# Performance work log

Hardware: AMD Instinct MI355X
Metric: run time of the kernel (lower is better)

## Reference

```python
import jax, jax.numpy as jnp
import numpy as np

K, S, P, NQ, NREPS = 3, 1, 1, 9, 2  # kernel, stride, pad, num_qubits, num_qreps


def _extract_patches(x, k, s):
    # x: (b, c, H, W) -> (b, c, ho, wo, k*k), patch elems in (kh, kw) row-major order
    b, c, H, W = x.shape
    ho = (H - k) // s + 1
    wo = (W - k) // s + 1
    cols = [x[:, :, i:i + (ho - 1) * s + 1:s, j:j + (wo - 1) * s + 1:s]
            for i in range(k) for j in range(k)]
    return jnp.stack(cols, axis=-1), ho, wo


def _cnot(state, c, t):
    # state: (N, 2, ..., 2); CNOT with control wire c, target wire t (wire q -> axis q+1)
    s0, s1 = jnp.split(state, 2, axis=c + 1)
    return jnp.concatenate([s0, jnp.flip(s1, axis=t + 1)], axis=c + 1)


def _simulate(angles, weights):
    # AngleEmbedding(RX) + BasicEntanglerLayers(RZ, CNOT ring) + expval(PauliY_i)
    # angles: (N, n) float; weights: (L, n) float -> (N, n) float expvals
    N, n = angles.shape
    half = 0.5 * angles
    # RX(theta)|0> = cos(t/2)|0> - i sin(t/2)|1>  (product state)
    vecs = jnp.stack([jnp.cos(half).astype(jnp.complex64),
                      -1j * jnp.sin(half)], axis=-1)  # (N, n, 2)
    state = vecs[:, 0]
    for q in range(1, n):
        state = state[..., None] * vecs[:, q].reshape((N,) + (1,) * q + (2,))
    # state: (N, 2, ..., 2), wire 0 = axis 1 (most significant)
    for l in range(weights.shape[0]):
        # RZ layer = single diagonal of shape (2,)*n, shared across patches
        pv = jnp.stack([jnp.exp(-0.5j * weights[l]),
                        jnp.exp(0.5j * weights[l])], axis=-1).astype(jnp.complex64)  # (n,2)
        diag = pv[0]
        for q in range(1, n):
            diag = diag[..., None] * pv[q].reshape((1,) * q + (2,))
        state = state * diag
        # CNOT ring (i -> i+1 mod n), as in BasicEntanglerLayers for n > 2
        for i in range(n):
            state = _cnot(state, i, (i + 1) % n)
    # <Y_i> = 2 * Im( sum conj(psi_{qi=0}) * psi_{qi=1} )
    exps = []
    for i in range(n):
        a, bdim = 1 << i, 1 << (n - 1 - i)
        r = state.reshape(N, a, 2, bdim)
        z = jnp.sum(jnp.conj(r[:, :, 0, :]) * r[:, :, 1, :], axis=(1, 2))
        exps.append(2.0 * z.imag)
    return jnp.stack(exps, axis=1)  # (N, n) float32


def setup_inputs() -> dict:
    key = jax.random.key(0)
    k1, k2 = jax.random.split(key)
    x = jax.random.uniform(k1, (16, 1, 28, 28), dtype=jnp.float32)
    weights = jax.random.uniform(k2, (NREPS, NQ), dtype=jnp.float32,
                                 minval=0.0, maxval=2.0 * np.pi)
    return {"x": x, "weights": weights}


def reference(x, weights):
    b = x.shape[0]
    xp = jnp.pad(x, ((0, 0), (0, 0), (P, P), (P, P)))
    patches, ho, wo = _extract_patches(xp, K, S)  # (b, 1, ho, wo, k*k)
    flat = patches.reshape(-1, NQ)                # (b*ho*wo, 9)  (c == 1)
    qout = _simulate(flat, weights)               # (b*ho*wo, 9)
    qout = qout.reshape(b, ho, wo, NQ)
    return qout.transpose(0, 3, 1, 2)             # (b, 9, ho, wo)
```

## Files before the change

kernel.cpp:

```cpp
#include <hip/hip_runtime.h>
#include <math.h>

#define NQ 9
#define NREPS 2
#define NB 512
#define NSIMS (16*28*28)

__host__ __device__ constexpr int csigma(int b) {
    for (int c = NQ - 1; c >= 0; --c) {
        const int t  = (c + 1) % NQ;
        const int pc = NQ - 1 - c;
        const int pt = NQ - 1 - t;
        b ^= ((b >> pc) & 1) << pt;
    }
    return b;
}
__host__ __device__ constexpr int csig2(int b) { return csigma(csigma(b)); }

constexpr int VB_[6] = { csig2(1<<0), csig2(1<<1), csig2(1<<2),
                         csig2(1<<3), csig2(1<<4), csig2(1<<5) };
constexpr int VR_[8] = { csig2(0<<6), csig2(1<<6), csig2(2<<6), csig2(3<<6),
                         csig2(4<<6), csig2(5<<6), csig2(6<<6), csig2(7<<6) };

template<int CTRL>
__device__ __forceinline__ float dppmov(float x) {
    return __int_as_float(__builtin_amdgcn_update_dpp(
        0, __float_as_int(x), CTRL, 0xF, 0xF, true));
}
template<int OFF>
__device__ __forceinline__ int swzx_i(int x) {
    return __builtin_amdgcn_ds_swizzle(x, OFF);
}
__device__ __forceinline__ float wave_reduce(float v) {
    v += dppmov<0x111>(v);
    v += dppmov<0x112>(v);
    v += dppmov<0x114>(v);
    v += dppmov<0x118>(v);
    v += dppmov<0x142>(v);
    v += dppmov<0x143>(v);
    return v;
}

typedef __fp16 h2_t __attribute__((ext_vector_type(2)));
__device__ __forceinline__ int packf16(float a, float b) {
    h2_t h = __builtin_amdgcn_cvt_pkrtz(a, b);
    int i; __builtin_memcpy(&i, &h, 4); return i;
}
__device__ __forceinline__ float2 unpackf16(int i) {
    h2_t h; __builtin_memcpy(&h, &i, 4);
    return make_float2((float)h.x, (float)h.y);
}

__global__ __launch_bounds__(256) void quanv_fused(
    const float* __restrict__ x,
    const float* __restrict__ w,
    float* __restrict__ out)
{
    __shared__ float2 T[NB];
    {
        const int t = threadIdx.x;
        #pragma unroll
        for (int bb = t; bb < NB; bb += 256) {
            float th = 0.f;
            int cur = bb;
            #pragma unroll
            for (int l = NREPS - 1; l >= 0; --l) {
                cur = csigma(cur);
                #pragma unroll
                for (int q = 0; q < NQ; ++q) {
                    const float wq = 0.5f * w[l * NQ + q];
                    th += ((cur >> (NQ - 1 - q)) & 1) ? wq : -wq;
                }
            }
            th -= 1.5707963267948966f * (float)__popc((unsigned)cur);
            float s, c;
            __sincosf(th, &s, &c);
            T[bb] = make_float2(c, s);
        }
    }
    __syncthreads();

    const int tid  = blockIdx.x * blockDim.x + threadIdx.x;
    const int lane = threadIdx.x & 63;
    const int sim  = tid >> 6;
    const int ox  = sim % 28;
    const int oy  = (sim / 28) % 28;
    const int img = sim / 784;

    float cq[NQ], sq[NQ];
    #pragma unroll
    for (int q = 0; q < NQ; ++q) {
        const int ky = q / 3, kx = q % 3;
        const int y  = oy + ky - 1;
        const int xx = ox + kx - 1;
        float a = 0.f;
        if (y >= 0 && y < 28 && xx >= 0 && xx < 28)
            a = x[img * 784 + y * 28 + xx];
        const float h = 0.5f * a;
        sq[q] = __sinf(h);
        cq[q] = __cosf(h);
    }

    const int VL = ((lane & 1)  ? VB_[0] : 0) ^ ((lane & 2)  ? VB_[1] : 0)
                 ^ ((lane & 4)  ? VB_[2] : 0) ^ ((lane & 8)  ? VB_[3] : 0)
                 ^ ((lane & 16) ? VB_[4] : 0) ^ ((lane & 32) ? VB_[5] : 0);

    float P0[NQ], P1[NQ];
    #pragma unroll
    for (int q = 0; q < NQ; ++q) {
        const bool bit = (VL >> (NQ - 1 - q)) & 1;
        P0[q] = bit ? sq[q] : cq[q];
        P1[q] = bit ? cq[q] : sq[q];
    }

    float fre[8], fim[8];
    int   pk[8];
    #pragma unroll
    for (int r = 0; r < 8; ++r) {
        float m = ((VR_[r] >> (NQ - 1)) & 1) ? P1[0] : P0[0];
        #pragma unroll
        for (int q = 1; q < NQ; ++q)
            m *= ((VR_[r] >> (NQ - 1 - q)) & 1) ? P1[q] : P0[q];
        const float2 t = T[(r << 6) | lane];
        fre[r] = m * t.x;
        fim[r] = m * t.y;
        pk[r]  = packf16(fre[r], fim[r]);
    }

    float e[NQ];

#define EXPQ_DPP(i, P, CTRL)                                       \
    {                                                              \
        const float sign = ((lane >> (P)) & 1) ? -1.f : 1.f;       \
        float acc = 0.f;                                           \
        _Pragma("unroll")                                          \
        for (int r = 0; r < 8; ++r) {                              \
            const float gre = dppmov<CTRL>(fre[r]);                \
            const float gim = dppmov<CTRL>(fim[r]);                \
            acc += fre[r] * gim - fim[r] * gre;                    \
        }                                                          \
        e[i] = sign * acc;                                         \
    }
    EXPQ_DPP(8, 0, 0xB1)
    EXPQ_DPP(7, 1, 0x4E)
    EXPQ_DPP(5, 3, 0x128)
#undef EXPQ_DPP

#define EXPQ_SWZ(i, P, OFF)                                        \
    {                                                              \
        const float sign = ((lane >> (P)) & 1) ? -1.f : 1.f;       \
        float acc = 0.f;                                           \
        _Pragma("unroll")                                          \
        for (int r = 0; r < 8; ++r) {                              \
            const float2 g = unpackf16(swzx_i<OFF>(pk[r]));        \
            acc += fre[r] * g.y - fim[r] * g.x;                    \
        }                                                          \
        e[i] = sign * acc;                                         \
    }
    EXPQ_SWZ(6, 2, 0x101F)
    EXPQ_SWZ(4, 4, 0x401F)
#undef EXPQ_SWZ

    {
        const float sign = ((lane >> 5) & 1) ? -1.f : 1.f;
        float acc = 0.f;
        #pragma unroll
        for (int r = 0; r < 8; ++r) {
            const float2 g = unpackf16(__shfl_xor(pk[r], 32, 64));
            acc += fre[r] * g.y - fim[r] * g.x;
        }
        e[3] = sign * acc;
    }

    #pragma unroll
    for (int i = 0; i < 3; ++i) {
        const int rb = 2 - i;
        float acc = 0.f;
        #pragma unroll
        for (int r = 0; r < 8; ++r) {
            if (!((r >> rb) & 1)) {
                const int r1 = r | (1 << rb);
                acc += fre[r] * fim[r1] - fim[r] * fre[r1];
            }
        }
        e[i] = 2.f * acc;
    }

    #pragma unroll
    for (int i = 0; i < NQ; ++i)
        e[i] = wave_reduce(e[i]);

    if (lane == 63) {
        float* o = out + img * (NQ * 784) + oy * 28 + ox;
        #pragma unroll
        for (int i = 0; i < NQ; ++i)
            o[i * 784] = e[i];
    }
}

extern "C" void kernel_launch(void* const* d_in, const int* in_sizes, int n_in,
                              void* d_out, int out_size, void* d_ws, size_t ws_size,
                              hipStream_t stream) {
    const float* x = (const float*)d_in[0];
    const float* w = (const float*)d_in[1];
    float* out = (float*)d_out;
    (void)d_ws; (void)ws_size; (void)in_sizes; (void)n_in; (void)out_size;

    quanv_fused<<<NSIMS / 4, 256, 0, stream>>>(x, w, out);
}
```

Measured before the change: 68.47 us.

## Split phase-table setup into separate kernel and factor amplitude products

Moves the per-block computation of the 512-entry RZ phase table into a one-block setup kernel that writes a global device array, which the main kernel then reads directly. This removes the per-block shared-memory fill and __syncthreads. Separately, the eight per-lane amplitude products are rebuilt from shared partial products of the P0/P1 factors, using static_asserts on the permutation structure, instead of nine multiplies each. The cost is an extra kernel launch and global rather than shared-memory reads of the table.

```diff
diff --git a/kernel.cpp b/kernel.cpp
--- a/kernel.cpp
+++ b/kernel.cpp
@@ -19,8 +19,31 @@
 
 constexpr int VB_[6] = { csig2(1<<0), csig2(1<<1), csig2(1<<2),
                          csig2(1<<3), csig2(1<<4), csig2(1<<5) };
-constexpr int VR_[8] = { csig2(0<<6), csig2(1<<6), csig2(2<<6), csig2(3<<6),
-                         csig2(4<<6), csig2(5<<6), csig2(6<<6), csig2(7<<6) };
+static_assert(csig2(1<<6) == ((1<<4)|(1<<6)), "G0");
+static_assert(csig2(1<<7) == ((1<<5)|(1<<7)), "G1");
+static_assert(csig2(1<<8) == ((1<<6)|(1<<8)), "G2");
+
+__device__ float2 g_T[NB];
+
+__global__ void quanv_setup(const float* __restrict__ w) {
+    const int b = threadIdx.x;
+    if (b >= NB) return;
+    float th = 0.f;
+    int cur = b;
+    #pragma unroll
+    for (int l = NREPS - 1; l >= 0; --l) {
+        cur = csigma(cur);
+        #pragma unroll
+        for (int q = 0; q < NQ; ++q) {
+            const float wq = 0.5f * w[l * NQ + q];
+            th += ((cur >> (NQ - 1 - q)) & 1) ? wq : -wq;
+        }
+    }
+    th -= 1.5707963267948966f * (float)__popc((unsigned)cur);
+    float s, c;
+    __sincosf(th, &s, &c);
+    g_T[b] = make_float2(c, s);
+}
 
 template<int CTRL>
 __device__ __forceinline__ float dppmov(float x) {
@@ -51,35 +74,10 @@
     return make_float2((float)h.x, (float)h.y);
 }
 
-__global__ __launch_bounds__(256) void quanv_fused(
+__global__ __launch_bounds__(256) void quanv_main(
     const float* __restrict__ x,
-    const float* __restrict__ w,
     float* __restrict__ out)
 {
-    __shared__ float2 T[NB];
-    {
-        const int t = threadIdx.x;
-        #pragma unroll
-        for (int bb = t; bb < NB; bb += 256) {
-            float th = 0.f;
-            int cur = bb;
-            #pragma unroll
-            for (int l = NREPS - 1; l >= 0; --l) {
-                cur = csigma(cur);
-                #pragma unroll
-                for (int q = 0; q < NQ; ++q) {
-                    const float wq = 0.5f * w[l * NQ + q];
-                    th += ((cur >> (NQ - 1 - q)) & 1) ? wq : -wq;
-                }
-            }
-            th -= 1.5707963267948966f * (float)__popc((unsigned)cur);
-            float s, c;
-            __sincosf(th, &s, &c);
-            T[bb] = make_float2(c, s);
-        }
-    }
-    __syncthreads();
-
     const int tid  = blockIdx.x * blockDim.x + threadIdx.x;
     const int lane = threadIdx.x & 63;
     const int sim  = tid >> 6;
@@ -113,15 +111,23 @@
         P1[q] = bit ? cq[q] : sq[q];
     }
 
+    const float K   = P0[5] * P0[6] * P0[7] * P0[8];
+    const float Fb0 = P0[3] * P0[1], Fb1 = P1[3] * P1[1];
+    const float T2_0 = K * Fb0, T2_1 = K * Fb1;
+    const float T24_00 = T2_0 * P0[0], T24_01 = T2_0 * P1[0];
+    const float T24_10 = T2_1 * P0[0], T24_11 = T2_1 * P1[0];
+    const float PP_00 = P0[4] * P0[2], PP_01 = P0[4] * P1[2];
+    const float PP_10 = P1[4] * P1[2], PP_11 = P1[4] * P0[2];
+    const float T24_[2][2] = { {T24_00, T24_01}, {T24_10, T24_11} };
+    const float PP_[2][2]  = { {PP_00, PP_01}, {PP_10, PP_11} };
+
     float fre[8], fim[8];
     int   pk[8];
     #pragma unroll
     for (int r = 0; r < 8; ++r) {
-        float m = ((VR_[r] >> (NQ - 1)) & 1) ? P1[0] : P0[0];
-        #pragma unroll
-        for (int q = 1; q < NQ; ++q)
-            m *= ((VR_[r] >> (NQ - 1 - q)) & 1) ? P1[q] : P0[q];
-        const float2 t = T[(r << 6) | lane];
+        const int p1 = r & 1, p2 = (r >> 1) & 1, p4 = (r >> 2) & 1;
+        const float m = T24_[p2][p4] * PP_[p1][p4];
+        const float2 t = g_T[(r << 6) | lane];
         fre[r] = m * t.x;
         fim[r] = m * t.y;
         pk[r]  = packf16(fre[r], fim[r]);
@@ -206,5 +212,6 @@
     float* out = (float*)d_out;
     (void)d_ws; (void)ws_size; (void)in_sizes; (void)n_in; (void)out_size;
 
-    quanv_fused<<<NSIMS / 4, 256, 0, stream>>>(x, w, out);
-}
+    quanv_setup<<<1, NB, 0, stream>>>(w);
+    quanv_main<<<NSIMS / 4, 256, 0, stream>>>(x, out);
+}
```

Result: no change. 68.11 us (-0.5%).
